# Optimization experiments

Hardware: AMD Instinct MI355X
Metric: run time of the kernel (lower is better)

Reference implementation:

```python
import jax, jax.numpy as jnp
import numpy as np

NUM_CLASSES = 10
GAMMA = 1.0
EPS = 1e-12


def setup_inputs() -> dict:
    key = jax.random.key(0)
    k1, k2, k3, k4 = jax.random.split(key, 4)
    x = jax.random.normal(k1, (1024, 64), dtype=jnp.float32)
    exemplars = jax.random.normal(k2, (50000, 64), dtype=jnp.float32)
    exemplar_labels = jax.random.randint(k3, (50000,), 0, NUM_CLASSES)
    # beta_raw initialized as softplus^{-1}(init_beta) with init_beta=1.0
    init_beta = 1.0
    beta_raw = jnp.array([np.log(np.exp(init_beta) - 1.0)], dtype=jnp.float32)
    return {"x": x, "exemplars": exemplars, "exemplar_labels": exemplar_labels,
            "beta_raw": beta_raw}


def reference(x, exemplars, exemplar_labels, beta_raw):
    # Squared Euclidean distances (weight_diag == ones) via GEMM expansion:
    # d2[b, e] = ||x_b||^2 + ||e_e||^2 - 2 <x_b, e_e>
    x2 = jnp.sum(x * x, axis=-1, keepdims=True)            # (B, 1)
    e2 = jnp.sum(exemplars * exemplars, axis=-1)           # (Ne,)
    d2 = x2 + e2[None, :] - 2.0 * (x @ exemplars.T)        # (B, Ne)
    d2 = jnp.maximum(d2, 0.0)  # true sq-dist is nonneg; guards GEMM round-off
    beta = jax.nn.softplus(beta_raw[0])
    sims = jnp.exp(-beta * d2)                              # (B, Ne)
    # scatter-add similarities into per-class bins: (C, B) -> (B, C)
    class_sims = jax.ops.segment_sum(sims.T, exemplar_labels,
                                     num_segments=NUM_CLASSES).T
    logits = GAMMA * jnp.log(class_sims + EPS)
    return logits
```

## Files before the change

### kernel.cpp

```cpp
#include <hip/hip_runtime.h>


#define NB      1024
#define NE      50000
#define NCHUNK  98
#define KD      64
#define NC      10
#define SROWS   64
#define NSTAGE  8
#define CROWS   512
#define LROW    72
#define BCOLS   256
#define NGRP    4

#define LOG2E   1.4426950408889634f

using half8   = __attribute__((ext_vector_type(8))) _Float16;
using half4v  = __attribute__((ext_vector_type(4))) _Float16;
using floatx4 = __attribute__((ext_vector_type(4))) float;

__device__ __forceinline__ float softplus_f(float x) {
  return (x > 20.f) ? x : log1pf(__expf(x));
}

__device__ __forceinline__ float exp2_hw(float x) {
#if __has_builtin(__builtin_amdgcn_exp2f)
  return __builtin_amdgcn_exp2f(x);
#else
  return exp2f(x);
#endif
}

__global__ __launch_bounds__(256) void main_kernel(
    const float* __restrict__ x, const float* __restrict__ ex,
    const int* __restrict__ labels, const float* __restrict__ beta_raw,
    float* __restrict__ part)
{
  __shared__ _Float16 Ah[2][SROWS * LROW];
  __shared__ float    Ce[2][SROWS];
  __shared__ int      Lb_all[CROWS];

  const int tid  = threadIdx.x;
  const int wave = tid >> 6;
  const int lane = tid & 63;
  const int l15  = lane & 15;
  const int quad = lane >> 4;

  const int btile = blockIdx.x;
  const int chunk = blockIdx.y;
  const int e0    = chunk * CROWS;
  const int bm0   = btile * BCOLS + wave * 16;

  const float beta = softplus_f(beta_raw[0]);
  const float nb2  = -beta * LOG2E;
  const float s2   = 2.f * beta * LOG2E;

  #pragma unroll
  for (int i = 0; i < CROWS / 256; ++i) {
    const int r = i * 256 + tid;
    const int grow = e0 + r;
    Lb_all[r] = (grow < NE) ? labels[grow] : 0;
  }

  half8 bx[NGRP][2];
  float cbl[NGRP];
  #pragma unroll
  for (int g = 0; g < NGRP; ++g) {
    const float* xr = x + (size_t)(bm0 + 64 * g + l15) * KD;
    const float4 v0 = *(const float4*)(xr + quad * 8);
    const float4 v1 = *(const float4*)(xr + quad * 8 + 4);
    const float4 v2 = *(const float4*)(xr + quad * 8 + 32);
    const float4 v3 = *(const float4*)(xr + quad * 8 + 36);
    bx[g][0] = half8{ (_Float16)v0.x, (_Float16)v0.y, (_Float16)v0.z, (_Float16)v0.w,
                      (_Float16)v1.x, (_Float16)v1.y, (_Float16)v1.z, (_Float16)v1.w };
    bx[g][1] = half8{ (_Float16)v2.x, (_Float16)v2.y, (_Float16)v2.z, (_Float16)v2.w,
                      (_Float16)v3.x, (_Float16)v3.y, (_Float16)v3.z, (_Float16)v3.w };
    float s = v0.x*v0.x + v0.y*v0.y + v0.z*v0.z + v0.w*v0.w
            + v1.x*v1.x + v1.y*v1.y + v1.z*v1.z + v1.w*v1.w
            + v2.x*v2.x + v2.y*v2.y + v2.z*v2.z + v2.w*v2.w
            + v3.x*v3.x + v3.y*v3.y + v3.z*v3.z + v3.w*v3.w;
    s += __shfl_xor(s, 16, 64);
    s += __shfl_xor(s, 32, 64);
    cbl[g] = nb2 * s;
  }

  const int srow = tid >> 2;
  const int scol = tid & 3;
  const int lofs = srow * LROW + scol * 16;

  float4 pf0, pf1, pf2, pf3;
  bool   pvalid;

  auto stage_load = [&](int st) {
    const int grow = e0 + st * SROWS + srow;
    pvalid = grow < NE;
    pf0 = make_float4(0.f, 0.f, 0.f, 0.f);
    pf1 = pf0; pf2 = pf0; pf3 = pf0;
    if (pvalid) {
      const float* g = ex + (size_t)grow * KD + scol * 16;
      pf0 = *(const float4*)(g);
      pf1 = *(const float4*)(g + 4);
      pf2 = *(const float4*)(g + 8);
      pf3 = *(const float4*)(g + 12);
    }
  };

  auto stage_write = [&](int buf) {
    float sn = pf0.x*pf0.x + pf0.y*pf0.y + pf0.z*pf0.z + pf0.w*pf0.w
             + pf1.x*pf1.x + pf1.y*pf1.y + pf1.z*pf1.z + pf1.w*pf1.w
             + pf2.x*pf2.x + pf2.y*pf2.y + pf2.z*pf2.z + pf2.w*pf2.w
             + pf3.x*pf3.x + pf3.y*pf3.y + pf3.z*pf3.z + pf3.w*pf3.w;
    sn += __shfl_xor(sn, 1, 64);
    sn += __shfl_xor(sn, 2, 64);
    const half8 h0 = { (_Float16)pf0.x, (_Float16)pf0.y, (_Float16)pf0.z, (_Float16)pf0.w,
                       (_Float16)pf1.x, (_Float16)pf1.y, (_Float16)pf1.z, (_Float16)pf1.w };
    const half8 h1 = { (_Float16)pf2.x, (_Float16)pf2.y, (_Float16)pf2.z, (_Float16)pf2.w,
                       (_Float16)pf3.x, (_Float16)pf3.y, (_Float16)pf3.z, (_Float16)pf3.w };
    *(half8*)(&Ah[buf][lofs])     = h0;
    *(half8*)(&Ah[buf][lofs + 8]) = h1;
    if (scol == 0) Ce[buf][srow] = pvalid ? (nb2 * sn) : -1e30f;
  };

  stage_load(0);
  stage_write(0);
  __syncthreads();

  floatx4 acc[NGRP];
  #pragma unroll
  for (int g = 0; g < NGRP; ++g) acc[g] = floatx4{0.f, 0.f, 0.f, 0.f};

  for (int st = 0; st < NSTAGE; ++st) {
    const int b = st & 1;

    if (st + 1 < NSTAGE) stage_load(st + 1);

    #pragma unroll
    for (int sub = 0; sub < 4; ++sub) {
      const int abase = (sub * 16 + l15) * LROW + quad * 8;
      const half8 ae0 = *(const half8*)(&Ah[b][abase]);
      const half8 ae1 = *(const half8*)(&Ah[b][abase + 32]);
      const float4 ce4 = *(const float4*)(&Ce[b][sub * 16 + quad * 4]);
      const int4   lb4 = *(const int4*)(&Lb_all[st * SROWS + sub * 16 + quad * 4]);

      floatx4 d[NGRP];
      #pragma unroll
      for (int g = 0; g < NGRP; ++g) {
        floatx4 t = {0.f, 0.f, 0.f, 0.f};
        t = __builtin_amdgcn_mfma_f32_16x16x32_f16(ae0, bx[g][0], t, 0, 0, 0);
        t = __builtin_amdgcn_mfma_f32_16x16x32_f16(ae1, bx[g][1], t, 0, 0, 0);
        d[g] = t;
      }

      const float cef[4] = { ce4.x, ce4.y, ce4.z, ce4.w };
      float t[NGRP][4];
      #pragma unroll
      for (int g = 0; g < NGRP; ++g)
        #pragma unroll
        for (int r = 0; r < 4; ++r)
          t[g][r] = fminf(fmaf(s2, d[g][r], cbl[g] + cef[r]), 0.f);

      float m = -1e30f;
      #pragma unroll
      for (int g = 0; g < NGRP; ++g)
        m = fmaxf(m, fmaxf(fmaxf(t[g][0], t[g][1]), fmaxf(t[g][2], t[g][3])));
      if (__any(m > -25.f)) {
        half4v oh;
        oh[0] = (lb4.x == l15) ? (_Float16)1.f : (_Float16)0.f;
        oh[1] = (lb4.y == l15) ? (_Float16)1.f : (_Float16)0.f;
        oh[2] = (lb4.z == l15) ? (_Float16)1.f : (_Float16)0.f;
        oh[3] = (lb4.w == l15) ? (_Float16)1.f : (_Float16)0.f;

        #pragma unroll
        for (int g = 0; g < NGRP; ++g) {
          half4v p;
          #pragma unroll
          for (int r = 0; r < 4; ++r) p[r] = (_Float16)exp2_hw(t[g][r]);
          acc[g] = __builtin_amdgcn_mfma_f32_16x16x16f16(oh, p, acc[g], 0, 0, 0);
        }
      }
    }

    if (st + 1 < NSTAGE) {
      stage_write((st + 1) & 1);
      __syncthreads();
    }
  }

  float* dst = part + (size_t)chunk * (NB * NC);
  #pragma unroll
  for (int r = 0; r < 4; ++r) {
    const int c = quad * 4 + r;
    if (c < NC) {
      #pragma unroll
      for (int g = 0; g < NGRP; ++g)
        dst[(bm0 + 64 * g + l15) * NC + c] = acc[g][r];
    }
  }
}

__global__ __launch_bounds__(256) void reduce_kernel(
    const float* __restrict__ part, float* __restrict__ out)
{
  const int bc = blockIdx.x * 256 + threadIdx.x;
  if (bc < NB * NC) {
    float s = 0.f;
    #pragma unroll 7
    for (int k = 0; k < NCHUNK; ++k) s += part[(size_t)k * (NB * NC) + bc];
    out[bc] = __logf(s + 1e-12f);
  }
}

extern "C" void kernel_launch(void* const* d_in, const int* in_sizes, int n_in,
                              void* d_out, int out_size, void* d_ws, size_t ws_size,
                              hipStream_t stream)
{
  const float* x        = (const float*)d_in[0];
  const float* ex       = (const float*)d_in[1];
  const int*   labels   = (const int*)d_in[2];
  const float* beta_raw = (const float*)d_in[3];
  float* out = (float*)d_out;

  float* part = (float*)d_ws;

  dim3 g(NB / BCOLS, NCHUNK);
  main_kernel<<<g, 256, 0, stream>>>(x, ex, labels, beta_raw, part);
  reduce_kernel<<<40, 256, 0, stream>>>(part, out);
}
```

Measured before the change: 94.65 us.

## Halve chunk size, add per-wave bound prefilter and skip dead partial writes

```diff
diff --git a/kernel.cpp b/kernel.cpp
--- a/kernel.cpp
+++ b/kernel.cpp
@@ -3,15 +3,16 @@
 
 #define NB      1024
 #define NE      50000
-#define NCHUNK  98
+#define NCHUNK  196
 #define KD      64
 #define NC      10
 #define SROWS   64
-#define NSTAGE  8
-#define CROWS   512
+#define NSTAGE  4
+#define CROWS   256
 #define LROW    72
 #define BCOLS   256
 #define NGRP    4
+#define NBT     (NB / BCOLS)
 
 #define LOG2E   1.4426950408889634f
 
@@ -34,11 +35,13 @@
 __global__ __launch_bounds__(256) void main_kernel(
     const float* __restrict__ x, const float* __restrict__ ex,
     const int* __restrict__ labels, const float* __restrict__ beta_raw,
-    float* __restrict__ part)
+    float* __restrict__ part, int* __restrict__ flags)
 {
   __shared__ _Float16 Ah[2][SROWS * LROW];
   __shared__ float    Ce[2][SROWS];
+  __shared__ float    CeMax[2][4];
   __shared__ int      Lb_all[CROWS];
+  __shared__ int      blockLive;
 
   const int tid  = threadIdx.x;
   const int wave = tid >> 6;
@@ -55,12 +58,11 @@
   const float nb2  = -beta * LOG2E;
   const float s2   = 2.f * beta * LOG2E;
 
-  #pragma unroll
-  for (int i = 0; i < CROWS / 256; ++i) {
-    const int r = i * 256 + tid;
-    const int grow = e0 + r;
-    Lb_all[r] = (grow < NE) ? labels[grow] : 0;
-  }
+  {
+    const int grow = e0 + tid;
+    Lb_all[tid] = (grow < NE) ? labels[grow] : 0;
+  }
+  if (tid == 0) blockLive = 0;
 
   half8 bx[NGRP][2];
   float cbl[NGRP];
@@ -112,13 +114,22 @@
              + pf3.x*pf3.x + pf3.y*pf3.y + pf3.z*pf3.z + pf3.w*pf3.w;
     sn += __shfl_xor(sn, 1, 64);
     sn += __shfl_xor(sn, 2, 64);
+    const float cev = pvalid ? (nb2 * sn) : -1e30f;
     const half8 h0 = { (_Float16)pf0.x, (_Float16)pf0.y, (_Float16)pf0.z, (_Float16)pf0.w,
                        (_Float16)pf1.x, (_Float16)pf1.y, (_Float16)pf1.z, (_Float16)pf1.w };
     const half8 h1 = { (_Float16)pf2.x, (_Float16)pf2.y, (_Float16)pf2.z, (_Float16)pf2.w,
                        (_Float16)pf3.x, (_Float16)pf3.y, (_Float16)pf3.z, (_Float16)pf3.w };
     *(half8*)(&Ah[buf][lofs])     = h0;
     *(half8*)(&Ah[buf][lofs + 8]) = h1;
-    if (scol == 0) Ce[buf][srow] = pvalid ? (nb2 * sn) : -1e30f;
+    if (scol == 0) Ce[buf][srow] = cev;
+    float cv = (scol == 0) ? cev : -1e30f;
+    cv = fmaxf(cv, __shfl_xor(cv, 1, 64));
+    cv = fmaxf(cv, __shfl_xor(cv, 2, 64));
+    cv = fmaxf(cv, __shfl_xor(cv, 4, 64));
+    cv = fmaxf(cv, __shfl_xor(cv, 8, 64));
+    cv = fmaxf(cv, __shfl_xor(cv, 16, 64));
+    cv = fmaxf(cv, __shfl_xor(cv, 32, 64));
+    if (lane == 0) CeMax[buf][wave] = cv;
   };
 
   stage_load(0);
@@ -139,8 +150,6 @@
       const int abase = (sub * 16 + l15) * LROW + quad * 8;
       const half8 ae0 = *(const half8*)(&Ah[b][abase]);
       const half8 ae1 = *(const half8*)(&Ah[b][abase + 32]);
-      const float4 ce4 = *(const float4*)(&Ce[b][sub * 16 + quad * 4]);
-      const int4   lb4 = *(const int4*)(&Lb_all[st * SROWS + sub * 16 + quad * 4]);
 
       floatx4 d[NGRP];
       #pragma unroll
@@ -151,31 +160,43 @@
         d[g] = t;
       }
 
-      const float cef[4] = { ce4.x, ce4.y, ce4.z, ce4.w };
-      float t[NGRP][4];
+      const float cemax = CeMax[b][sub];
+      float tbm = -1e30f;
       #pragma unroll
-      for (int g = 0; g < NGRP; ++g)
+      for (int g = 0; g < NGRP; ++g) {
+        const float dm = fmaxf(fmaxf(d[g][0], d[g][1]), fmaxf(d[g][2], d[g][3]));
+        tbm = fmaxf(tbm, fmaf(s2, dm, cbl[g] + cemax));
+      }
+      if (__any(tbm > -25.f)) {
+        const float4 ce4 = *(const float4*)(&Ce[b][sub * 16 + quad * 4]);
+        const int4   lb4 = *(const int4*)(&Lb_all[st * SROWS + sub * 16 + quad * 4]);
+        const float cef[4] = { ce4.x, ce4.y, ce4.z, ce4.w };
+
+        float t[NGRP][4];
         #pragma unroll
-        for (int r = 0; r < 4; ++r)
-          t[g][r] = fminf(fmaf(s2, d[g][r], cbl[g] + cef[r]), 0.f);
-
-      float m = -1e30f;
-      #pragma unroll
-      for (int g = 0; g < NGRP; ++g)
-        m = fmaxf(m, fmaxf(fmaxf(t[g][0], t[g][1]), fmaxf(t[g][2], t[g][3])));
-      if (__any(m > -25.f)) {
-        half4v oh;
-        oh[0] = (lb4.x == l15) ? (_Float16)1.f : (_Float16)0.f;
-        oh[1] = (lb4.y == l15) ? (_Float16)1.f : (_Float16)0.f;
-        oh[2] = (lb4.z == l15) ? (_Float16)1.f : (_Float16)0.f;
-        oh[3] = (lb4.w == l15) ? (_Float16)1.f : (_Float16)0.f;
-
+        for (int g = 0; g < NGRP; ++g)
+          #pragma unroll
+          for (int r = 0; r < 4; ++r)
+            t[g][r] = fminf(fmaf(s2, d[g][r], cbl[g] + cef[r]), 0.f);
+
+        float m = -1e30f;
         #pragma unroll
-        for (int g = 0; g < NGRP; ++g) {
-          half4v p;
+        for (int g = 0; g < NGRP; ++g)
+          m = fmaxf(m, fmaxf(fmaxf(t[g][0], t[g][1]), fmaxf(t[g][2], t[g][3])));
+        if (__any(m > -25.f)) {
+          half4v oh;
+          oh[0] = (lb4.x == l15) ? (_Float16)1.f : (_Float16)0.f;
+          oh[1] = (lb4.y == l15) ? (_Float16)1.f : (_Float16)0.f;
+          oh[2] = (lb4.z == l15) ? (_Float16)1.f : (_Float16)0.f;
+          oh[3] = (lb4.w == l15) ? (_Float16)1.f : (_Float16)0.f;
+
           #pragma unroll
-          for (int r = 0; r < 4; ++r) p[r] = (_Float16)exp2_hw(t[g][r]);
-          acc[g] = __builtin_amdgcn_mfma_f32_16x16x16f16(oh, p, acc[g], 0, 0, 0);
+          for (int g = 0; g < NGRP; ++g) {
+            half4v p;
+            #pragma unroll
+            for (int r = 0; r < 4; ++r) p[r] = (_Float16)exp2_hw(t[g][r]);
+            acc[g] = __builtin_amdgcn_mfma_f32_16x16x16f16(oh, p, acc[g], 0, 0, 0);
+          }
         }
       }
     }
@@ -186,26 +207,42 @@
     }
   }
 
-  float* dst = part + (size_t)chunk * (NB * NC);
+  bool ll = false;
   #pragma unroll
-  for (int r = 0; r < 4; ++r) {
-    const int c = quad * 4 + r;
-    if (c < NC) {
-      #pragma unroll
-      for (int g = 0; g < NGRP; ++g)
-        dst[(bm0 + 64 * g + l15) * NC + c] = acc[g][r];
-    }
-  }
+  for (int g = 0; g < NGRP; ++g)
+    #pragma unroll
+    for (int r = 0; r < 4; ++r) ll |= (acc[g][r] != 0.f);
+  __syncthreads();
+  if (__any(ll) && lane == 0) blockLive = 1;
+  __syncthreads();
+
+  if (blockLive) {
+    float* dst = part + (size_t)chunk * (NB * NC);
+    #pragma unroll
+    for (int r = 0; r < 4; ++r) {
+      const int c = quad * 4 + r;
+      if (c < NC) {
+        #pragma unroll
+        for (int g = 0; g < NGRP; ++g)
+          dst[(bm0 + 64 * g + l15) * NC + c] = acc[g][r];
+      }
+    }
+  }
+  if (tid == 0) flags[btile * NCHUNK + chunk] = blockLive;
 }
 
 __global__ __launch_bounds__(256) void reduce_kernel(
-    const float* __restrict__ part, float* __restrict__ out)
+    const float* __restrict__ part, const int* __restrict__ flags,
+    float* __restrict__ out)
 {
   const int bc = blockIdx.x * 256 + threadIdx.x;
   if (bc < NB * NC) {
+    const int btile = bc / (BCOLS * NC);
+    const int fbase = btile * NCHUNK;
     float s = 0.f;
-    #pragma unroll 7
-    for (int k = 0; k < NCHUNK; ++k) s += part[(size_t)k * (NB * NC) + bc];
+    for (int k = 0; k < NCHUNK; ++k) {
+      if (flags[fbase + k]) s += part[(size_t)k * (NB * NC) + bc];
+    }
     out[bc] = __logf(s + 1e-12f);
   }
 }
@@ -220,9 +257,11 @@
   const float* beta_raw = (const float*)d_in[3];
   float* out = (float*)d_out;
 
-  float* part = (float*)d_ws;
-
-  dim3 g(NB / BCOLS, NCHUNK);
-  main_kernel<<<g, 256, 0, stream>>>(x, ex, labels, beta_raw, part);
-  reduce_kernel<<<40, 256, 0, stream>>>(part, out);
-}
+  char* ws = (char*)d_ws;
+  float* part  = (float*)ws;
+  int*   flags = (int*)(ws + (size_t)NCHUNK * NB * NC * 4);
+
+  dim3 g(NBT, NCHUNK);
+  main_kernel<<<g, 256, 0, stream>>>(x, ex, labels, beta_raw, part, flags);
+  reduce_kernel<<<40, 256, 0, stream>>>(part, flags, out);
+}
```

Measured after the change: 103.4 us. 1.09x slower.
